# Kernel tuning notes

Hardware: AMD Instinct MI355X
Metric: run time of the kernel (lower is better)

## Reference

```python
import jax, jax.numpy as jnp
import numpy as np

B, T, E, H = 2, 2048, 1024, 16
D = E // H


def setup_inputs() -> dict:
    key = jax.random.key(0)
    ks = jax.random.split(key, 8)
    k = jax.random.normal(ks[0], (B, T, E), dtype=jnp.float32)
    q = jax.random.normal(ks[1], (B, T, E), dtype=jnp.float32)
    v = jax.random.normal(ks[2], (B, T, E), dtype=jnp.float32)
    # torch Linear weights: [out, in]; y = x @ W.T (+ b)
    Wk = jax.random.normal(ks[3], (E, E), dtype=jnp.float32) * 0.02
    Wq = jax.random.normal(ks[4], (E, E), dtype=jnp.float32) * 0.02
    Wv = jax.random.normal(ks[5], (E, E), dtype=jnp.float32) * 0.02
    Wo = jax.random.normal(ks[6], (E, E), dtype=jnp.float32) * 0.02
    bo = jax.random.normal(ks[7], (E,), dtype=jnp.float32) * 0.02
    # causal mask: True = masked (as in masked_fill)
    mask = jnp.triu(jnp.ones((T, T), dtype=bool), k=1)
    return {"k": k, "q": q, "v": v, "Wk": Wk, "Wq": Wq, "Wv": Wv,
            "Wo": Wo, "bo": bo, "mask": mask}


def _split_heads(x):  # [b,t,(h d)] -> [b,h,t,d]
    b, t, _ = x.shape
    return x.reshape(b, t, H, D).transpose(0, 2, 1, 3)


def reference(k, q, v, Wk, Wq, Wv, Wo, bo, mask):
    keys = _split_heads(k @ Wk.T)      # no bias (add_bias_kv=False)
    queries = _split_heads(q @ Wq.T)   # q_prj has bias=False always
    values = _split_heads(v @ Wv.T)
    # scores [b,h,t,t]; original applies mask (-inf) then divides by sqrt(d)
    att = jnp.einsum('bhqd,bhkd->bhqk', queries, keys)
    att = jnp.where(mask, -jnp.inf, att)
    att = jax.nn.softmax(att / jnp.sqrt(jnp.float32(D)), axis=-1)
    out = jnp.einsum('bhqk,bhkd->bhqd', att, values)
    out = out.transpose(0, 2, 1, 3).reshape(B, T, E)  # merge heads
    return out @ Wo.T + bo
```

## Files before the change

### kernel.cpp

```cpp
#include <hip/hip_runtime.h>
#include <stdint.h>

typedef __bf16 bf16;
typedef bf16 bf16x8 __attribute__((ext_vector_type(8)));
typedef bf16 bf16x4 __attribute__((ext_vector_type(4)));
typedef float f32x4 __attribute__((ext_vector_type(4)));
typedef float f32x16 __attribute__((ext_vector_type(16)));
typedef unsigned int uint;
typedef uint u32x4 __attribute__((ext_vector_type(4)));

#define MFMA16(a, b, c) __builtin_amdgcn_mfma_f32_16x16x32_bf16(a, b, c, 0, 0, 0)
#define MFMA32(a, b, c) __builtin_amdgcn_mfma_f32_32x32x16_bf16(a, b, c, 0, 0, 0)

static constexpr int Bsz = 2, T = 2048, E = 1024, H = 16, Dh = 64;
static constexpr float QSCALE = 0.125f * 1.44269504088896f;

__device__ __forceinline__ float exp2fast(float x) {
#if __has_builtin(__builtin_amdgcn_exp2f)
    return __builtin_amdgcn_exp2f(x);
#else
    return exp2f(x);
#endif
}

__device__ __forceinline__ void gll16(const bf16* g, bf16* l) {
    __builtin_amdgcn_global_load_lds((const __attribute__((address_space(1))) uint*)g,
                                     (__attribute__((address_space(3))) uint*)l, 16, 0, 0);
}

template <int ROWS>
__device__ __forceinline__ void stage_b16(bf16* lds, const bf16* g, int ldg, int wave, int lane) {
    const int rsub = lane >> 3;
    const int csw = (lane & 7) ^ rsub;
#pragma unroll
    for (int i = 0; i < ROWS / 32; ++i) {
        const int row = wave * (ROWS / 4) + i * 8;
        gll16(g + (size_t)(row + rsub) * ldg + csw * 8, lds + row * 64);
    }
}
__device__ __forceinline__ bf16x8 frag_b16(const bf16* lds, int r, int cc) {
    return *(const bf16x8*)(lds + r * 64 + ((cc ^ (r & 7)) << 3));
}

template <int ROWS>
__device__ __forceinline__ void stage_f32lds(float* lds, const float* g, int ldg,
                                             int wave, int lane) {
    const int rsub = lane >> 4;
#pragma unroll
    for (int i = 0; i < ROWS / 16; ++i) {
        const int slab = wave * (ROWS / 16) + i;
        const int row0 = slab * 4;
        const int src = (lane & 15) ^ ((((slab & 3)) << 2) | rsub);
        gll16((const bf16*)(g + (size_t)(row0 + rsub) * ldg + src * 4),
              (bf16*)(lds + row0 * 64));
    }
}
__device__ __forceinline__ bf16x8 frag_f32(const float* lds, int r, int lc0) {
    const f32x4 u0 = *(const f32x4*)(lds + r * 64 + ((lc0 ^ (r & 15)) << 2));
    const f32x4 u1 = *(const f32x4*)(lds + r * 64 + (((lc0 + 1) ^ (r & 15)) << 2));
    bf16x8 a = {(bf16)u0.x, (bf16)u0.y, (bf16)u0.z, (bf16)u0.w,
                (bf16)u1.x, (bf16)u1.y, (bf16)u1.z, (bf16)u1.w};
    return a;
}

template <int MF, int NF, bool OUTF32>
__device__ __forceinline__ void gemm_dbuf(bf16* smem, const bf16* A, const bf16* B,
                                          bf16* Yb, float* Yf, const float* bias,
                                          int m0, int n0, int K, int ldy, float oscale) {
    constexpr int BM = MF * 32, BN = NF * 32;
    constexpr int ABUF = BM * 64, SET = ABUF + BN * 64;
    const int tid = threadIdx.x, lane = tid & 63, wave = tid >> 6;
    const int wm = wave >> 1, wn = wave & 1;
    const int fr = lane & 15, kg16 = lane >> 4;

    f32x4 acc[MF][NF] = {};

    stage_b16<BM>(smem, A + (size_t)m0 * K, K, wave, lane);
    stage_b16<BN>(smem + ABUF, B + (size_t)n0 * K, K, wave, lane);

    const int NS = K / 64;
    int cur = 0;
#pragma unroll 1
    for (int s = 0; s < NS; ++s) {
        if (s + 1 < NS) {
            bf16* dst = smem + (cur ^ 1) * SET;
            stage_b16<BM>(dst, A + (size_t)m0 * K + (s + 1) * 64, K, wave, lane);
            stage_b16<BN>(dst + ABUF, B + (size_t)n0 * K + (s + 1) * 64, K, wave, lane);
            if constexpr (MF + NF == 8)
                asm volatile("s_waitcnt vmcnt(8)" ::: "memory");
            else
                asm volatile("s_waitcnt vmcnt(6)" ::: "memory");
        } else {
            asm volatile("s_waitcnt vmcnt(0)" ::: "memory");
        }
        __builtin_amdgcn_s_barrier();
        asm volatile("" ::: "memory");

        const bf16* At = smem + cur * SET;
        const bf16* Bt = At + ABUF;
#pragma unroll
        for (int kk = 0; kk < 64; kk += 32) {
            bf16x8 af[MF], bfr[NF];
#pragma unroll
            for (int f = 0; f < MF; ++f)
                af[f] = frag_b16(At, wm * (BM / 2) + f * 16 + fr, (kk >> 3) + kg16);
#pragma unroll
            for (int f = 0; f < NF; ++f)
                bfr[f] = frag_b16(Bt, wn * (BN / 2) + f * 16 + fr, (kk >> 3) + kg16);
            __builtin_amdgcn_s_setprio(1);
#pragma unroll
            for (int mf = 0; mf < MF; ++mf)
#pragma unroll
                for (int nf = 0; nf < NF; ++nf)
                    acc[mf][nf] = MFMA16(af[mf], bfr[nf], acc[mf][nf]);
            __builtin_amdgcn_s_setprio(0);
        }
        asm volatile("" ::: "memory");
        __builtin_amdgcn_s_barrier();
        cur ^= 1;
    }
    const int rb = (lane >> 4) << 2;
#pragma unroll
    for (int mf = 0; mf < MF; ++mf)
#pragma unroll
        for (int nf = 0; nf < NF; ++nf) {
            int n = n0 + wn * (BN / 2) + nf * 16 + fr;
            float bn = 0.f;
            if constexpr (OUTF32) bn = bias[n];
#pragma unroll
            for (int r = 0; r < 4; ++r) {
                int mm = m0 + wm * (BM / 2) + mf * 16 + rb + r;
                float v = acc[mf][nf][r];
                if constexpr (OUTF32)
                    Yf[(size_t)mm * ldy + n] = v + bn;
                else
                    Yb[(size_t)mm * ldy + n] = (bf16)(v * oscale);
            }
        }
}

template <bool AF32, bool BF32, int MF, int NF, bool OUTF32>
__device__ __forceinline__ void gemm_body(char* smem, const void* Ap, const void* Bp,
                                          bf16* Yb, float* Yf, const float* bias,
                                          int m0, int n0, int K, int ldy, float oscale) {
    constexpr int BM = MF * 32, BN = NF * 32;
    constexpr int ASZ = BM * 64 * (AF32 ? 4 : 2);
    const int tid = threadIdx.x, lane = tid & 63, wave = tid >> 6;
    const int wm = wave >> 1, wn = wave & 1;
    const int fr = lane & 15, kg16 = lane >> 4;
    f32x4 acc[MF][NF] = {};
    for (int k0 = 0; k0 < K; k0 += 64) {
        if constexpr (AF32)
            stage_f32lds<BM>((float*)smem, (const float*)Ap + (size_t)m0 * K + k0, K, wave, lane);
        else
            stage_b16<BM>((bf16*)smem, (const bf16*)Ap + (size_t)m0 * K + k0, K, wave, lane);
        if constexpr (BF32)
            stage_f32lds<BN>((float*)(smem + ASZ), (const float*)Bp + (size_t)n0 * K + k0,
                             K, wave, lane);
        else
            stage_b16<BN>((bf16*)(smem + ASZ), (const bf16*)Bp + (size_t)n0 * K + k0,
                          K, wave, lane);
        __syncthreads();
#pragma unroll
        for (int kk = 0; kk < 64; kk += 32) {
            bf16x8 af[MF], bfr[NF];
#pragma unroll
            for (int f = 0; f < MF; ++f) {
                const int r = wm * (BM / 2) + f * 16 + fr;
                if constexpr (AF32)
                    af[f] = frag_f32((const float*)smem, r, (kk >> 2) + (kg16 << 1));
                else
                    af[f] = frag_b16((const bf16*)smem, r, (kk >> 3) + kg16);
            }
#pragma unroll
            for (int f = 0; f < NF; ++f) {
                const int r = wn * (BN / 2) + f * 16 + fr;
                if constexpr (BF32)
                    bfr[f] = frag_f32((const float*)(smem + ASZ), r, (kk >> 2) + (kg16 << 1));
                else
                    bfr[f] = frag_b16((const bf16*)(smem + ASZ), r, (kk >> 3) + kg16);
            }
#pragma unroll
            for (int mf = 0; mf < MF; ++mf)
#pragma unroll
                for (int nf = 0; nf < NF; ++nf)
                    acc[mf][nf] = MFMA16(af[mf], bfr[nf], acc[mf][nf]);
        }
        __syncthreads();
    }
    const int rb = (lane >> 4) << 2;
#pragma unroll
    for (int mf = 0; mf < MF; ++mf)
#pragma unroll
        for (int nf = 0; nf < NF; ++nf) {
            int n = n0 + wn * (BN / 2) + nf * 16 + fr;
            float bn = 0.f;
            if constexpr (OUTF32) bn = bias[n];
#pragma unroll
            for (int r = 0; r < 4; ++r) {
                int mm = m0 + wm * (BM / 2) + mf * 16 + rb + r;
                float v = acc[mf][nf][r];
                if constexpr (OUTF32)
                    Yf[(size_t)mm * ldy + n] = v + bn;
                else
                    Yb[(size_t)mm * ldy + n] = (bf16)(v * oscale);
            }
        }
}

__global__ __launch_bounds__(256) void cvt_qk(const float* q, const float* k,
                                              const float* Wq, const float* Wk,
                                              bf16* qc, bf16* kc, bf16* Wqc, bf16* Wkc) {
    const size_t NX = (size_t)Bsz * T * E, NW = (size_t)E * E;
    const size_t n1 = NX, n2 = 2 * NX, n3 = 2 * NX + NW, tot = (2 * NX + 2 * NW) >> 2;
    for (size_t t = (size_t)blockIdx.x * 256 + threadIdx.x; t < tot;
         t += (size_t)gridDim.x * 256) {
        size_t i = t << 2;
        const float* s;
        bf16* d;
        size_t off;
        if (i < n1) { s = q; d = qc; off = i; }
        else if (i < n2) { s = k; d = kc; off = i - n1; }
        else if (i < n3) { s = Wq; d = Wqc; off = i - n2; }
        else { s = Wk; d = Wkc; off = i - n3; }
        const float4 x = *(const float4*)(s + off);
        bf16x4 y = {(bf16)x.x, (bf16)x.y, (bf16)x.z, (bf16)x.w};
        *(bf16x4*)(d + off) = y;
    }
}
__global__ __launch_bounds__(256) void cvt_vw(const float* v, const float* Wv, const float* Wo,
                                              bf16* vc, bf16* Wvc, bf16* Woc) {
    const size_t NX = (size_t)Bsz * T * E, NW = (size_t)E * E;
    const size_t n1 = NX, n2 = NX + NW, tot = (NX + 2 * NW) >> 2;
    for (size_t t = (size_t)blockIdx.x * 256 + threadIdx.x; t < tot;
         t += (size_t)gridDim.x * 256) {
        size_t i = t << 2;
        const float* s;
        bf16* d;
        size_t off;
        if (i < n1) { s = v; d = vc; off = i; }
        else if (i < n2) { s = Wv; d = Wvc; off = i - n1; }
        else { s = Wo; d = Woc; off = i - n2; }
        const float4 x = *(const float4*)(s + off);
        bf16x4 y = {(bf16)x.x, (bf16)x.y, (bf16)x.z, (bf16)x.w};
        *(bf16x4*)(d + off) = y;
    }
}

__global__ __launch_bounds__(256) void proj_qk(const bf16* qc, const bf16* kc,
                                               const bf16* Wqc, const bf16* Wkc,
                                               bf16* Qb, bf16* Kb) {
    __shared__ __align__(16) bf16 smem[2 * (128 * 64 + 128 * 64)];
    const int bid = blockIdx.x;
    const int wid = (bid & 7) * 64 + (bid >> 3);
    const int s = wid >> 8;
    const int t = wid & 255;
    const int m0 = (t >> 3) * 128, n0 = (t & 7) * 128;
    gemm_dbuf<4, 4, false>(smem, s ? kc : qc, s ? Wkc : Wqc, s ? Kb : Qb,
                           nullptr, nullptr, m0, n0, E, E, s ? 1.0f : QSCALE);
}
__global__ __launch_bounds__(256) void proj_v(const bf16* Wvc, const bf16* vc, bf16* Vt) {
    __shared__ __align__(16) bf16 smem[2 * (128 * 64 + 128 * 64)];
    const int bid = blockIdx.x;
    const int wid = (bid & 7) * 32 + (bid >> 3);
    const int b = wid >> 7, rr = wid & 127;
    const int m0 = (rr >> 4) * 128, n0 = (rr & 15) * 128;
    gemm_dbuf<4, 4, false>(smem, Wvc, vc + (size_t)b * T * E, Vt + (size_t)b * E * T,
                           nullptr, nullptr, m0, n0, E, T, 1.0f);
}
__global__ __launch_bounds__(256) void out_proj_db(const bf16* Xb, const bf16* W16,
                                                   float* Y, const float* bias) {
    __shared__ __align__(16) bf16 smem[2 * (64 * 64 + 128 * 64)];
    const int bid = blockIdx.x;
    const int wid = (bid & 7) * 64 + (bid >> 3);
    const int m0 = (wid >> 3) * 64, n0 = (wid & 7) * 128;
    gemm_dbuf<2, 4, true>(smem, Xb, W16, nullptr, Y, bias, m0, n0, E, E, 1.0f);
}

__global__ __launch_bounds__(256) void qkv_proj_fb(
    const float* q32, const float* k32, const float* v32,
    const float* Wq32, const float* Wk32, const float* Wv32,
    bf16* Qb, bf16* Kb, bf16* Vt) {
    __shared__ __align__(16) char smem[64 * 1024];
    const int bid = blockIdx.x;
    const int wid = (bid & 7) * 96 + (bid >> 3);
    if (wid < 512) {
        int s = wid >> 8;
        int t = wid & 255;
        int m0 = (t >> 3) * 128, n0 = (t & 7) * 128;
        gemm_body<true, true, 4, 4, false>(smem, s ? k32 : q32, s ? Wk32 : Wq32,
                                           s ? Kb : Qb, nullptr, nullptr, m0, n0, E, E,
                                           s ? 1.0f : QSCALE);
    } else {
        int r = wid - 512;
        int b = r >> 7, rr = r & 127;
        int m0 = (rr >> 4) * 128, n0 = (rr & 15) * 128;
        gemm_body<true, true, 4, 4, false>(smem, Wv32, v32 + (size_t)b * T * E,
                                           Vt + (size_t)b * E * T, nullptr, nullptr,
                                           m0, n0, E, T, 1.0f);
    }
}
__global__ __launch_bounds__(256) void out_proj_fb(const bf16* Xb, const float* W32,
                                                   float* Y, const float* bias) {
    __shared__ __align__(16) char smem[40 * 1024];
    const int bid = blockIdx.x;
    const int wid = (bid & 7) * 64 + (bid >> 3);
    const int m0 = (wid >> 3) * 64, n0 = (wid & 7) * 128;
    gemm_body<false, true, 2, 4, true>(smem, Xb, W32, nullptr, Y, bias, m0, n0, E, E, 1.0f);
}

__device__ __forceinline__ uint pkbf(float a, float b) {
    uint16_t x = __builtin_bit_cast(uint16_t, (bf16)a);
    uint16_t y = __builtin_bit_cast(uint16_t, (bf16)b);
    return (uint)x | ((uint)y << 16);
}

template <int DMODE>
__device__ __forceinline__ void attn_tile64(const bf16* KL, const bf16* VL,
                                            int l31, int hi, int swz,
                                            const bf16x8 (&qf)[4],
                                            f32x16& o0, f32x16& o1, float& m, float& l) {
    constexpr int NCC = (DMODE == 2) ? 2 : 4;
    f32x16 s0 = {}, s1 = {};
    {
        bf16x8 kf[4];
#pragma unroll
        for (int t = 0; t < 4; ++t)
            kf[t] = *(const bf16x8*)(KL + l31 * 64 + ((((t << 1) | hi) ^ swz) << 3));
        __builtin_amdgcn_s_setprio(1);
#pragma unroll
        for (int t = 0; t < 4; ++t) s0 = MFMA32(kf[t], qf[t], s0);
        __builtin_amdgcn_s_setprio(0);
    }
    if constexpr (DMODE != 2) {
        bf16x8 kf[4];
#pragma unroll
        for (int t = 0; t < 4; ++t)
            kf[t] = *(const bf16x8*)(KL + (32 + l31) * 64 + ((((t << 1) | hi) ^ swz) << 3));
        __builtin_amdgcn_s_setprio(1);
#pragma unroll
        for (int t = 0; t < 4; ++t) s1 = MFMA32(kf[t], qf[t], s1);
        __builtin_amdgcn_s_setprio(0);
    }
    bf16x8 vfa[NCC], vfb[NCC];
#pragma unroll
    for (int cc = 0; cc < NCC; ++cc) {
        vfa[cc] = *(const bf16x8*)(VL + l31 * 64 + ((((cc << 1) | hi) ^ swz) << 3));
        vfb[cc] = *(const bf16x8*)(VL + (32 + l31) * 64 + ((((cc << 1) | hi) ^ swz) << 3));
    }
    if constexpr (DMODE == 2) {
#pragma unroll
        for (int r = 0; r < 16; ++r) {
            int key = (r & 3) + 8 * (r >> 2) + 4 * hi;
            if (key > l31) s0[r] = -1e30f;
        }
    }
    if constexpr (DMODE == 1) {
#pragma unroll
        for (int r = 0; r < 16; ++r) {
            int key = (r & 3) + 8 * (r >> 2) + 4 * hi;
            if (key > l31) s1[r] = -1e30f;
        }
    }
    float t8[8];
    if constexpr (DMODE == 2) {
#pragma unroll
        for (int r = 0; r < 8; ++r) t8[r] = fmaxf(s0[r], s0[r + 8]);
    } else {
#pragma unroll
        for (int r = 0; r < 8; ++r)
            t8[r] = fmaxf(fmaxf(s0[r], s0[r + 8]), fmaxf(s1[r], s1[r + 8]));
    }
#pragma unroll
    for (int r = 0; r < 4; ++r) t8[r] = fmaxf(t8[r], t8[r + 4]);
    float pm = fmaxf(fmaxf(t8[0], t8[1]), fmaxf(t8[2], t8[3]));
    pm = fmaxf(pm, __shfl_xor(pm, 32, 64));

    if (!__all(pm - m <= 11.5f)) {
        float mn = fmaxf(m, pm);
        float al = exp2fast(m - mn);
        m = mn;
        l *= al;
#pragma unroll
        for (int r = 0; r < 16; ++r) {
            int qr = (r & 3) + 8 * (r >> 2) + 4 * hi;
            float aq = __shfl(al, qr, 64);
            o0[r] *= aq;
            o1[r] *= aq;
        }
    }
#pragma unroll
    for (int r = 0; r < 16; ++r) s0[r] = exp2fast(s0[r] - m);
    if constexpr (DMODE != 2) {
#pragma unroll
        for (int r = 0; r < 16; ++r) s1[r] = exp2fast(s1[r] - m);
    }
    float u8[8];
    if constexpr (DMODE == 2) {
#pragma unroll
        for (int r = 0; r < 8; ++r) u8[r] = s0[r] + s0[r + 8];
    } else {
#pragma unroll
        for (int r = 0; r < 8; ++r) u8[r] = (s0[r] + s0[r + 8]) + (s1[r] + s1[r + 8]);
    }
#pragma unroll
    for (int r = 0; r < 4; ++r) u8[r] = u8[r] + u8[r + 4];
    float ps = (u8[0] + u8[1]) + (u8[2] + u8[3]);
    l += ps + __shfl_xor(ps, 32, 64);

    __builtin_amdgcn_s_setprio(1);
#pragma unroll
    for (int cc = 0; cc < NCC; ++cc) {
        const f32x16& ph = (cc < 2) ? s0 : s1;
        const int bse = (cc & 1) * 8;
        uint x0 = pkbf(ph[bse + 0], ph[bse + 1]);
        uint x1 = pkbf(ph[bse + 2], ph[bse + 3]);
        uint y0 = pkbf(ph[bse + 4], ph[bse + 5]);
        uint y1 = pkbf(ph[bse + 6], ph[bse + 7]);
        uint sx0 = __shfl_xor(x0, 32, 64), sx1 = __shfl_xor(x1, 32, 64);
        uint sy0 = __shfl_xor(y0, 32, 64), sy1 = __shfl_xor(y1, 32, 64);
        u32x4 wv;
        wv.x = hi ? sy0 : x0;
        wv.y = hi ? sy1 : x1;
        wv.z = hi ? y0 : sx0;
        wv.w = hi ? y1 : sx1;
        bf16x8 pa = __builtin_bit_cast(bf16x8, wv);
        o0 = MFMA32(pa, vfa[cc], o0);
        o1 = MFMA32(pa, vfb[cc], o1);
    }
    __builtin_amdgcn_s_setprio(0);
}

__global__ __launch_bounds__(256) void attn_fwd(const bf16* __restrict__ Q,
                                                const bf16* __restrict__ K,
                                                const bf16* __restrict__ Vt,
                                                bf16* __restrict__ O) {
    __shared__ __align__(16) bf16 Kl[2][64 * 64];
    __shared__ __align__(16) bf16 Vl[2][64 * 64];

    const int g = blockIdx.x;
    const int lo = g & 255;
    const int xcd = lo & 7, jj = lo >> 3;
    const int hb = xcd * 4 + (jj & 3);
    const int qhi = 15 - (jj >> 2);
    const int qb = (g < 256) ? qhi : 15 - qhi;
    const int h = hb & 15, b = hb >> 4;

    const int tid = threadIdx.x, lane = tid & 63, w = tid >> 6;
    const int l31 = lane & 31, hi = lane >> 5;
    const int q0 = qb * 128 + w * 32;

    const bf16* Qp = Q + (size_t)b * T * E + h * Dh;
    const bf16* Kp = K + (size_t)b * T * E + h * Dh;
    const bf16* Vp = Vt + ((size_t)b * E + h * Dh) * T;

    const int rsub = lane >> 3;
    const int csw = (lane & 7) ^ rsub;
    const int swz = (l31 & 7);

    bf16x8 qf[4];
#pragma unroll
    for (int t = 0; t < 4; ++t)
        qf[t] = *(const bf16x8*)(Qp + (size_t)(q0 + l31) * E + t * 16 + hi * 8);

    f32x16 o0 = {}, o1 = {};
    float m = -1e30f, l = 0.f;
    const int ktD = 2 * qb + (w >> 1);
    const int nK2 = 2 * qb + 2;

#pragma unroll
    for (int ii = 0; ii < 2; ++ii)
        gll16(Kp + (size_t)(16 * w + 8 * ii + rsub) * E + csw * 8, &Kl[0][(2 * w + ii) * 512]);
#pragma unroll
    for (int ii = 0; ii < 2; ++ii)
        gll16(Vp + (size_t)(16 * w + 8 * ii + rsub) * T + csw * 8, &Vl[0][(2 * w + ii) * 512]);

    int cur = 0;
#pragma unroll 1
    for (int K2 = 0; K2 < nK2; ++K2) {
        if (K2 + 1 < nK2) {
            const int kb = (K2 + 1) * 64;
            const bf16* Kg = Kp + (size_t)kb * E;
            const bf16* Vg = Vp + kb;
            bf16* dK = &Kl[cur ^ 1][0];
            bf16* dV = &Vl[cur ^ 1][0];
#pragma unroll
            for (int ii = 0; ii < 2; ++ii)
                gll16(Kg + (size_t)(16 * w + 8 * ii + rsub) * E + csw * 8, dK + (2 * w + ii) * 512);
#pragma unroll
            for (int ii = 0; ii < 2; ++ii)
                gll16(Vg + (size_t)(16 * w + 8 * ii + rsub) * T + csw * 8, dV + (2 * w + ii) * 512);
            asm volatile("s_waitcnt vmcnt(4)" ::: "memory");
        } else {
            asm volatile("s_waitcnt vmcnt(0)" ::: "memory");
        }
        __builtin_amdgcn_s_barrier();
        asm volatile("" ::: "memory");

        const bf16* KL = &Kl[cur][0];
        const bf16* VL = &Vl[cur][0];
        if (K2 < ktD) {
            attn_tile64<0>(KL, VL, l31, hi, swz, qf, o0, o1, m, l);
        } else if (K2 == ktD) {
            if (w & 1)
                attn_tile64<1>(KL, VL, l31, hi, swz, qf, o0, o1, m, l);
            else
                attn_tile64<2>(KL, VL, l31, hi, swz, qf, o0, o1, m, l);
        }
        asm volatile("" ::: "memory");
        __builtin_amdgcn_s_barrier();
        cur ^= 1;
    }

    bf16* Op = O + (size_t)b * T * E + h * Dh;
#pragma unroll
    for (int r = 0; r < 16; ++r) {
        int qr = (r & 3) + 8 * (r >> 2) + 4 * hi;
        float lq = __shfl(l, qr, 64);
        float inv = 1.0f / lq;
        Op[(size_t)(q0 + qr) * E + l31] = (bf16)(o0[r] * inv);
        Op[(size_t)(q0 + qr) * E + 32 + l31] = (bf16)(o1[r] * inv);
    }
}

extern "C" void kernel_launch(void* const* d_in, const int* in_sizes, int n_in,
                              void* d_out, int out_size, void* d_ws, size_t ws_size,
                              hipStream_t stream) {
    const float* k_in = (const float*)d_in[0];
    const float* q_in = (const float*)d_in[1];
    const float* v_in = (const float*)d_in[2];
    const float* Wk = (const float*)d_in[3];
    const float* Wq = (const float*)d_in[4];
    const float* Wv = (const float*)d_in[5];
    const float* Wo = (const float*)d_in[6];
    const float* bo = (const float*)d_in[7];
    float* out = (float*)d_out;

    const size_t NE = (size_t)Bsz * T * E;
    const size_t NW = (size_t)E * E;
    bf16* ws = (bf16*)d_ws;
    bf16* Qb = ws;
    bf16* Kb = ws + NE;
    bf16* Vt = ws + 2 * NE;
    bf16* Ab = ws + 3 * NE;
    bf16* Wqc = ws + 4 * NE;
    bf16* Wkc = Wqc + NW;
    bf16* Wvc = Wkc + NW;
    bf16* Woc = Wvc + NW;

    const bool planB = ws_size >= (4 * NE + 4 * NW) * sizeof(bf16);

    if (planB) {
        bf16* qc = Ab;
        bf16* kc = Vt;
        bf16* vc = Ab;
        cvt_qk<<<1024, 256, 0, stream>>>(q_in, k_in, Wq, Wk, qc, kc, Wqc, Wkc);
        proj_qk<<<512, 256, 0, stream>>>(qc, kc, Wqc, Wkc, Qb, Kb);
        cvt_vw<<<1024, 256, 0, stream>>>(v_in, Wv, Wo, vc, Wvc, Woc);
        proj_v<<<256, 256, 0, stream>>>(Wvc, vc, Vt);
        attn_fwd<<<dim3(512), 256, 0, stream>>>(Qb, Kb, Vt, Ab);
        out_proj_db<<<512, 256, 0, stream>>>(Ab, Woc, out, bo);
    } else {
        qkv_proj_fb<<<768, 256, 0, stream>>>(q_in, k_in, v_in, Wq, Wk, Wv, Qb, Kb, Vt);
        attn_fwd<<<dim3(512), 256, 0, stream>>>(Qb, Kb, Vt, Ab);
        out_proj_fb<<<512, 256, 0, stream>>>(Ab, Wo, out, bo);
    }
}
```

Measured before the change: 124.1 us.

## Fuse activation fp32→bf16 conversion into QKV projection GEMM staging

Activations are no longer converted to bf16 in separate passes. The projection GEMM now stages the fp32 activation tiles directly into LDS and converts them to bf16 when building MFMA fragments, and Q, K and V projections run in a single launch with smaller tiles. Only the weights are still pre-converted, by one kernel. This removes a full fp32 read plus bf16 write and re-read of the activations, along with two launches. The costs are double the LDS footprint for fp32 tiles, conversion work inside the inner loop, and the smaller tiles give less reuse per block.

```diff
diff --git a/kernel.cpp b/kernel.cpp
--- a/kernel.cpp
+++ b/kernel.cpp
@@ -63,50 +63,82 @@
     return a;
 }
 
-template <int MF, int NF, bool OUTF32>
-__device__ __forceinline__ void gemm_dbuf(bf16* smem, const bf16* A, const bf16* B,
-                                          bf16* Yb, float* Yf, const float* bias,
-                                          int m0, int n0, int K, int ldy, float oscale) {
+template <bool AF32, bool BF32, int MF, int NF, bool OUTF32>
+__device__ __forceinline__ void gemm_dbuf2(char* smem, const void* Ap, const void* Bp,
+                                           bf16* Yb, float* Yf, const float* bias,
+                                           int m0, int n0, int K, int ldy, float oscale) {
     constexpr int BM = MF * 32, BN = NF * 32;
-    constexpr int ABUF = BM * 64, SET = ABUF + BN * 64;
+    constexpr int ASZ = BM * 64 * (AF32 ? 4 : 2);
+    constexpr int SET = ASZ + BN * 64 * (BF32 ? 4 : 2);
+    constexpr int LD = (AF32 ? BM / 16 : BM / 32) + (BF32 ? BN / 16 : BN / 32);
     const int tid = threadIdx.x, lane = tid & 63, wave = tid >> 6;
     const int wm = wave >> 1, wn = wave & 1;
     const int fr = lane & 15, kg16 = lane >> 4;
 
+    const float* A32 = (const float*)Ap;
+    const bf16* A16 = (const bf16*)Ap;
+    const float* B32 = (const float*)Bp;
+    const bf16* B16 = (const bf16*)Bp;
+
     f32x4 acc[MF][NF] = {};
 
-    stage_b16<BM>(smem, A + (size_t)m0 * K, K, wave, lane);
-    stage_b16<BN>(smem + ABUF, B + (size_t)n0 * K, K, wave, lane);
+    auto stageA = [&](char* dst, int k0) {
+        if constexpr (AF32)
+            stage_f32lds<BM>((float*)dst, A32 + (size_t)m0 * K + k0, K, wave, lane);
+        else
+            stage_b16<BM>((bf16*)dst, A16 + (size_t)m0 * K + k0, K, wave, lane);
+    };
+    auto stageB = [&](char* dst, int k0) {
+        if constexpr (BF32)
+            stage_f32lds<BN>((float*)dst, B32 + (size_t)n0 * K + k0, K, wave, lane);
+        else
+            stage_b16<BN>((bf16*)dst, B16 + (size_t)n0 * K + k0, K, wave, lane);
+    };
+
+    stageA(smem, 0);
+    stageB(smem + ASZ, 0);
 
     const int NS = K / 64;
     int cur = 0;
 #pragma unroll 1
     for (int s = 0; s < NS; ++s) {
         if (s + 1 < NS) {
-            bf16* dst = smem + (cur ^ 1) * SET;
-            stage_b16<BM>(dst, A + (size_t)m0 * K + (s + 1) * 64, K, wave, lane);
-            stage_b16<BN>(dst + ABUF, B + (size_t)n0 * K + (s + 1) * 64, K, wave, lane);
-            if constexpr (MF + NF == 8)
+            char* dst = smem + (cur ^ 1) * SET;
+            stageA(dst, (s + 1) * 64);
+            stageB(dst + ASZ, (s + 1) * 64);
+            if constexpr (LD == 8)
                 asm volatile("s_waitcnt vmcnt(8)" ::: "memory");
+            else if constexpr (LD == 6)
+                asm volatile("s_waitcnt vmcnt(6)" ::: "memory");
             else
-                asm volatile("s_waitcnt vmcnt(6)" ::: "memory");
+                asm volatile("s_waitcnt vmcnt(0)" ::: "memory");
         } else {
             asm volatile("s_waitcnt vmcnt(0)" ::: "memory");
         }
         __builtin_amdgcn_s_barrier();
         asm volatile("" ::: "memory");
 
-        const bf16* At = smem + cur * SET;
-        const bf16* Bt = At + ABUF;
+        const char* At = smem + cur * SET;
+        const char* Bt = At + ASZ;
 #pragma unroll
         for (int kk = 0; kk < 64; kk += 32) {
             bf16x8 af[MF], bfr[NF];
 #pragma unroll
-            for (int f = 0; f < MF; ++f)
-                af[f] = frag_b16(At, wm * (BM / 2) + f * 16 + fr, (kk >> 3) + kg16);
-#pragma unroll
-            for (int f = 0; f < NF; ++f)
-                bfr[f] = frag_b16(Bt, wn * (BN / 2) + f * 16 + fr, (kk >> 3) + kg16);
+            for (int f = 0; f < MF; ++f) {
+                const int r = wm * (BM / 2) + f * 16 + fr;
+                if constexpr (AF32)
+                    af[f] = frag_f32((const float*)At, r, (kk >> 2) + (kg16 << 1));
+                else
+                    af[f] = frag_b16((const bf16*)At, r, (kk >> 3) + kg16);
+            }
+#pragma unroll
+            for (int f = 0; f < NF; ++f) {
+                const int r = wn * (BN / 2) + f * 16 + fr;
+                if constexpr (BF32)
+                    bfr[f] = frag_f32((const float*)Bt, r, (kk >> 2) + (kg16 << 1));
+                else
+                    bfr[f] = frag_b16((const bf16*)Bt, r, (kk >> 3) + kg16);
+            }
             __builtin_amdgcn_s_setprio(1);
 #pragma unroll
             for (int mf = 0; mf < MF; ++mf)
@@ -208,73 +240,55 @@
         }
 }
 
-__global__ __launch_bounds__(256) void cvt_qk(const float* q, const float* k,
-                                              const float* Wq, const float* Wk,
-                                              bf16* qc, bf16* kc, bf16* Wqc, bf16* Wkc) {
-    const size_t NX = (size_t)Bsz * T * E, NW = (size_t)E * E;
-    const size_t n1 = NX, n2 = 2 * NX, n3 = 2 * NX + NW, tot = (2 * NX + 2 * NW) >> 2;
-    for (size_t t = (size_t)blockIdx.x * 256 + threadIdx.x; t < tot;
+__global__ __launch_bounds__(256) void cvt_w(const float* Wq, const float* Wk,
+                                             const float* Wv, const float* Wo,
+                                             bf16* Wqc, bf16* Wkc, bf16* Wvc, bf16* Woc) {
+    const size_t NW = (size_t)E * E;
+    const size_t nwork = (4 * NW) >> 2;
+    for (size_t t = (size_t)blockIdx.x * 256 + threadIdx.x; t < nwork;
          t += (size_t)gridDim.x * 256) {
         size_t i = t << 2;
-        const float* s;
-        bf16* d;
-        size_t off;
-        if (i < n1) { s = q; d = qc; off = i; }
-        else if (i < n2) { s = k; d = kc; off = i - n1; }
-        else if (i < n3) { s = Wq; d = Wqc; off = i - n2; }
-        else { s = Wk; d = Wkc; off = i - n3; }
+        size_t w = i / NW;
+        size_t off = i - w * NW;
+        const float* s = w == 0 ? Wq : (w == 1 ? Wk : (w == 2 ? Wv : Wo));
+        bf16* d = w == 0 ? Wqc : (w == 1 ? Wkc : (w == 2 ? Wvc : Woc));
         const float4 x = *(const float4*)(s + off);
         bf16x4 y = {(bf16)x.x, (bf16)x.y, (bf16)x.z, (bf16)x.w};
         *(bf16x4*)(d + off) = y;
     }
 }
-__global__ __launch_bounds__(256) void cvt_vw(const float* v, const float* Wv, const float* Wo,
-                                              bf16* vc, bf16* Wvc, bf16* Woc) {
-    const size_t NX = (size_t)Bsz * T * E, NW = (size_t)E * E;
-    const size_t n1 = NX, n2 = NX + NW, tot = (NX + 2 * NW) >> 2;
-    for (size_t t = (size_t)blockIdx.x * 256 + threadIdx.x; t < tot;
-         t += (size_t)gridDim.x * 256) {
-        size_t i = t << 2;
-        const float* s;
-        bf16* d;
-        size_t off;
-        if (i < n1) { s = v; d = vc; off = i; }
-        else if (i < n2) { s = Wv; d = Wvc; off = i - n1; }
-        else { s = Wo; d = Woc; off = i - n2; }
-        const float4 x = *(const float4*)(s + off);
-        bf16x4 y = {(bf16)x.x, (bf16)x.y, (bf16)x.z, (bf16)x.w};
-        *(bf16x4*)(d + off) = y;
-    }
-}
-
-__global__ __launch_bounds__(256) void proj_qk(const bf16* qc, const bf16* kc,
-                                               const bf16* Wqc, const bf16* Wkc,
-                                               bf16* Qb, bf16* Kb) {
-    __shared__ __align__(16) bf16 smem[2 * (128 * 64 + 128 * 64)];
+
+__global__ __launch_bounds__(256) void proj_qkv(
+    const float* q32, const float* k32, const float* v32,
+    const bf16* Wqc, const bf16* Wkc, const bf16* Wvc,
+    bf16* Qb, bf16* Kb, bf16* Vt) {
+    __shared__ __align__(16) char smem[64 * 1024];
     const int bid = blockIdx.x;
-    const int wid = (bid & 7) * 64 + (bid >> 3);
-    const int s = wid >> 8;
-    const int t = wid & 255;
-    const int m0 = (t >> 3) * 128, n0 = (t & 7) * 128;
-    gemm_dbuf<4, 4, false>(smem, s ? kc : qc, s ? Wkc : Wqc, s ? Kb : Qb,
-                           nullptr, nullptr, m0, n0, E, E, s ? 1.0f : QSCALE);
-}
-__global__ __launch_bounds__(256) void proj_v(const bf16* Wvc, const bf16* vc, bf16* Vt) {
-    __shared__ __align__(16) bf16 smem[2 * (128 * 64 + 128 * 64)];
-    const int bid = blockIdx.x;
-    const int wid = (bid & 7) * 32 + (bid >> 3);
-    const int b = wid >> 7, rr = wid & 127;
-    const int m0 = (rr >> 4) * 128, n0 = (rr & 15) * 128;
-    gemm_dbuf<4, 4, false>(smem, Wvc, vc + (size_t)b * T * E, Vt + (size_t)b * E * T,
-                           nullptr, nullptr, m0, n0, E, T, 1.0f);
-}
+    const int wid = (bid & 7) * 192 + (bid >> 3);
+    if (wid < 1024) {
+        const int s = wid >> 9;
+        const int t = wid & 511;
+        const int m0 = (t >> 3) * 64, n0 = (t & 7) * 128;
+        gemm_dbuf2<true, false, 2, 4, false>(smem, s ? k32 : q32, s ? Wkc : Wqc,
+                                             s ? Kb : Qb, nullptr, nullptr, m0, n0, E, E,
+                                             s ? 1.0f : QSCALE);
+    } else {
+        const int r = wid - 1024;
+        const int b = r >> 8, rr = r & 255;
+        const int m0 = (rr >> 5) * 128, n0 = (rr & 31) * 64;
+        gemm_dbuf2<false, true, 4, 2, false>(smem, Wvc, v32 + (size_t)b * T * E,
+                                             Vt + (size_t)b * E * T, nullptr, nullptr,
+                                             m0, n0, E, T, 1.0f);
+    }
+}
+
 __global__ __launch_bounds__(256) void out_proj_db(const bf16* Xb, const bf16* W16,
                                                    float* Y, const float* bias) {
-    __shared__ __align__(16) bf16 smem[2 * (64 * 64 + 128 * 64)];
+    __shared__ __align__(16) char smem[48 * 1024];
     const int bid = blockIdx.x;
     const int wid = (bid & 7) * 64 + (bid >> 3);
     const int m0 = (wid >> 3) * 64, n0 = (wid & 7) * 128;
-    gemm_dbuf<2, 4, true>(smem, Xb, W16, nullptr, Y, bias, m0, n0, E, E, 1.0f);
+    gemm_dbuf2<false, false, 2, 4, true>(smem, Xb, W16, nullptr, Y, bias, m0, n0, E, E, 1.0f);
 }
 
 __global__ __launch_bounds__(256) void qkv_proj_fb(
@@ -551,13 +565,8 @@
     const bool planB = ws_size >= (4 * NE + 4 * NW) * sizeof(bf16);
 
     if (planB) {
-        bf16* qc = Ab;
-        bf16* kc = Vt;
-        bf16* vc = Ab;
-        cvt_qk<<<1024, 256, 0, stream>>>(q_in, k_in, Wq, Wk, qc, kc, Wqc, Wkc);
-        proj_qk<<<512, 256, 0, stream>>>(qc, kc, Wqc, Wkc, Qb, Kb);
-        cvt_vw<<<1024, 256, 0, stream>>>(v_in, Wv, Wo, vc, Wvc, Woc);
-        proj_v<<<256, 256, 0, stream>>>(Wvc, vc, Vt);
+        cvt_w<<<512, 256, 0, stream>>>(Wq, Wk, Wv, Wo, Wqc, Wkc, Wvc, Woc);
+        proj_qkv<<<1536, 256, 0, stream>>>(q_in, k_in, v_in, Wqc, Wkc, Wvc, Qb, Kb, Vt);
         attn_fwd<<<dim3(512), 256, 0, stream>>>(Qb, Kb, Vt, Ab);
         out_proj_db<<<512, 256, 0, stream>>>(Ab, Woc, out, bo);
     } else {
```

After: 122.9 us. Within noise of the previous version (-1.0%).
